# Performance work log

Measured on AMD Instinct MI355X. Metric: run time of the kernel, lower is better.

## Reference

```python
import jax, jax.numpy as jnp
import numpy as np
from jax import lax

B, C_IN, C_OUT, RES, K = 2, 16, 32, 64, 3


def setup_inputs() -> dict:
    key = jax.random.key(0)
    kx, km, kw = jax.random.split(key, 3)
    x = jax.random.normal(kx, (B, C_IN, RES, RES, RES), dtype=jnp.float32)
    # the rest are exactly zero -> drives the nonzero-voxel masking path
    keep = jax.random.bernoulli(km, 0.3, (B, 1, RES, RES, RES))
    x = x * keep.astype(jnp.float32)
    # weight matches nn.Parameter(torch.randn(1, out_ch, in_ch, k, k, k))
    weight = jax.random.normal(kw, (1, C_OUT, C_IN, K, K, K), dtype=jnp.float32)
    return {"x": x, "weight": weight}


def reference(x, weight):
    # SparseConv3d: output at voxel v (for each out channel) is
    #   sum_{i, dx, dy, dz} padded_x[i, v+offset] * W[o, i, offset+pad]
    # evaluated ONLY where x has any nonzero channel; zero elsewhere.
    # This is a 'same'-padded cross-correlation masked by voxel occupancy.
    w = weight[0]  # [O, I, k, k, k]
    out = lax.conv_general_dilated(
        x, w,
        window_strides=(1, 1, 1),
        padding="SAME",
        dimension_numbers=("NCDHW", "OIDHW", "NCDHW"),
    )  # [B, O, D, H, W]
    occ = jnp.any(x != 0, axis=1, keepdims=True)  # [B,1,D,H,W] nonzero-voxel mask
    return out * occ.astype(out.dtype)
```

## Files before the change

kernel.cpp:

```cpp
#include <hip/hip_runtime.h>

#define RES   64
#define RES2  4096
#define RES3  262144
#define CIN   16
#define COUT  32
#define NWH (27*CIN*COUT)

#define ROWB  1088
#define XT_BYTES (72*ROWB)
#define LDS_BYTES XT_BYTES

typedef _Float16 f16x8 __attribute__((ext_vector_type(8)));
typedef float   f32x16 __attribute__((ext_vector_type(16)));

static __device__ __forceinline__ unsigned int pack2(float v0, float v1) {
    _Float16 h0 = (_Float16)v0;
    _Float16 h1 = (_Float16)v1;
    unsigned short u0 = __builtin_bit_cast(unsigned short, h0);
    unsigned short u1 = __builtin_bit_cast(unsigned short, h1);
    return (unsigned int)u0 | ((unsigned int)u1 << 16);
}

__global__ __launch_bounds__(256) void wtrans_kernel(
    const float* __restrict__ w, _Float16* __restrict__ wtg) {
    int i = blockIdx.x * 256 + threadIdx.x;
    if (i >= NWH) return;
    int tap = i >> 9;
    int hi  = (i >> 8) & 1;
    int o   = (i >> 3) & 31;
    int c   = i & 7;
    wtg[i] = (_Float16)w[(o * CIN + hi * 8 + c) * 27 + tap];
}

__global__ __launch_bounds__(512, 4) void conv_kernel(
    const float* __restrict__ x, const char* __restrict__ wtgb,
    float* __restrict__ out) {

    extern __shared__ char smem[];
    char* xt = smem;

    int bid = blockIdx.x;
    int sb  = (bid & 7) * 64 + (bid >> 3);
    int b   = sb >> 8;
    int zt  = (sb >> 4) & 15;
    int yt  = sb & 15;
    int z0 = zt * 4, y0 = yt * 4;

    int tid  = threadIdx.x;
    int lane = tid & 63;
    int wv   = tid >> 6;
    int hi   = lane >> 5;
    int l31  = lane & 31;

    const float* xb = x + (size_t)b * CIN * RES3;
    const uint4 zz = make_uint4(0u, 0u, 0u, 0u);
    #pragma unroll
    for (int j = 0; j < 5; ++j) {
        int p = wv + j * 8;
        if (p >= 36) break;
        int iz = p / 6, iy = p - iz * 6;
        int gz = z0 + iz - 1, gy = y0 + iy - 1;
        char* d0 = xt + (p * 2) * ROWB;
        uint4 lo = zz, hh = zz;
        if (((unsigned)gz < 64u) && ((unsigned)gy < 64u)) {
            const float* sp = xb + gz * RES2 + gy * RES + lane;
            float v0  = sp[0];          float v1  = sp[RES3];
            float v2  = sp[2 * RES3];   float v3  = sp[3 * RES3];
            float v4  = sp[4 * RES3];   float v5  = sp[5 * RES3];
            float v6  = sp[6 * RES3];   float v7  = sp[7 * RES3];
            float v8  = sp[8 * RES3];   float v9  = sp[9 * RES3];
            float v10 = sp[10 * RES3];  float v11 = sp[11 * RES3];
            float v12 = sp[12 * RES3];  float v13 = sp[13 * RES3];
            float v14 = sp[14 * RES3];  float v15 = sp[15 * RES3];
            lo = make_uint4(pack2(v0, v1),  pack2(v2, v3),
                            pack2(v4, v5),  pack2(v6, v7));
            hh = make_uint4(pack2(v8, v9),  pack2(v10, v11),
                            pack2(v12, v13), pack2(v14, v15));
        }
        *(uint4*)(d0 + (lane + 1) * 16)        = lo;
        *(uint4*)(d0 + ROWB + (lane + 1) * 16) = hh;
        if (lane < 4) {
            int cz = (lane == 0) ? 0 : (64 + lane);
            *(uint4*)(d0 + cz * 16)        = zz;
            *(uint4*)(d0 + ROWB + cz * 16) = zz;
        }
    }
    __syncthreads();

    int oy  = wv & 3;
    int oz0 = (wv >> 2) * 2;

    const char* xbase = xt + hi * ROWB + l31 * 16;
    const char* wtab  = wtgb + hi * 512 + l31 * 16;

    f32x16 acc00 = {};
    f32x16 acc01 = {};
    f32x16 acc10 = {};
    f32x16 acc11 = {};

    #pragma unroll
    for (int g = 0; g < 3; ++g) {
        #pragma unroll
        for (int dyp = 0; dyp < 3; ++dyp) {
            const char* wp = wtab + (size_t)(g * 9 + dyp * 3) * 1024;
            f16x8 wf0 = *(const f16x8*)(wp);
            f16x8 wf1 = *(const f16x8*)(wp + 1024);
            f16x8 wf2 = *(const f16x8*)(wp + 2048);
            const char* xrow = xbase + (((oz0 + g) * 6 + (oy + dyp)) * 2) * ROWB;
            #pragma unroll
            for (int dxp = 0; dxp < 3; ++dxp) {
                f16x8 wf = (dxp == 0) ? wf0 : ((dxp == 1) ? wf1 : wf2);
                f16x8 bA0 = *(const f16x8*)(xrow + dxp * 16);
                f16x8 bA1 = *(const f16x8*)(xrow + 512 + dxp * 16);
                f16x8 bB0 = *(const f16x8*)(xrow + 12 * ROWB + dxp * 16);
                f16x8 bB1 = *(const f16x8*)(xrow + 12 * ROWB + 512 + dxp * 16);
                acc00 = __builtin_amdgcn_mfma_f32_32x32x16_f16(wf, bA0, acc00, 0, 0, 0);
                acc01 = __builtin_amdgcn_mfma_f32_32x32x16_f16(wf, bA1, acc01, 0, 0, 0);
                acc10 = __builtin_amdgcn_mfma_f32_32x32x16_f16(wf, bB0, acc10, 0, 0, 0);
                acc11 = __builtin_amdgcn_mfma_f32_32x32x16_f16(wf, bB1, acc11, 0, 0, 0);
            }
        }
    }

    unsigned occm[2][2];
    #pragma unroll
    for (int ozo = 0; ozo < 2; ++ozo) {
        int R = (((oz0 + ozo + 1) * 6) + (oy + 1)) * 2;
        #pragma unroll
        for (int xh = 0; xh < 2; ++xh) {
            const char* mp = xt + R * ROWB + (xh * 32 + l31 + 1) * 16;
            uint4 a = *(const uint4*)(mp);
            uint4 c = *(const uint4*)(mp + ROWB);
            occm[ozo][xh] = (a.x | a.y | a.z | a.w | c.x | c.y | c.z | c.w) & 0x7FFF7FFFu;
        }
    }
    bool oA0 = occm[0][0] != 0u, oA1 = occm[0][1] != 0u;
    bool oB0 = occm[1][0] != 0u, oB1 = occm[1][1] != 0u;

    size_t vaddrA = (size_t)(z0 + oz0) * RES2 + (y0 + oy) * RES + l31;
    size_t vaddrB = vaddrA + RES2;

    #pragma unroll
    for (int r = 0; r < 16; ++r) {
        int o = (r & 3) + 8 * (r >> 2) + 4 * hi;
        float* pl = out + ((size_t)(b * COUT + o) << 18);
        pl[vaddrA]      = oA0 ? acc00[r] : 0.0f;
        pl[vaddrA + 32] = oA1 ? acc01[r] : 0.0f;
        pl[vaddrB]      = oB0 ? acc10[r] : 0.0f;
        pl[vaddrB + 32] = oB1 ? acc11[r] : 0.0f;
    }
}

extern "C" void kernel_launch(void* const* d_in, const int* in_sizes, int n_in,
                              void* d_out, int out_size, void* d_ws, size_t ws_size,
                              hipStream_t stream) {
    const float* x = (const float*)d_in[0];
    const float* w = (const float*)d_in[1];
    float* out = (float*)d_out;

    _Float16* wtg = (_Float16*)d_ws;

    (void)hipFuncSetAttribute(reinterpret_cast<const void*>(conv_kernel),
                              hipFuncAttributeMaxDynamicSharedMemorySize, LDS_BYTES);

    wtrans_kernel<<<(NWH + 255) / 256, 256, 0, stream>>>(w, wtg);
    conv_kernel<<<512, 512, LDS_BYTES, stream>>>(x, (const char*)wtg, out);
}
```

Before: 101.9 us.

## Halve z-tile per block, preload all weights to registers, raise occupancy

Each block now covers 2 z-slices instead of 4, so the grid doubles to 1024 blocks and LDS per block shrinks to 48 rows. Each wave computes one output row with two accumulators instead of four. All 27 weight fragments are loaded into registers up front, and the MFMA loop runs at raised wave priority. Launch bounds go up to 6 blocks per CU to improve occupancy and latency hiding. The cost is more halo reloading, since each z-slice's input is staged by more blocks, and higher register pressure from the preloaded weights.

```diff
diff --git a/kernel.cpp b/kernel.cpp
--- a/kernel.cpp
+++ b/kernel.cpp
@@ -8,7 +8,7 @@
 #define NWH (27*CIN*COUT)
 
 #define ROWB  1088
-#define XT_BYTES (72*ROWB)
+#define XT_BYTES (48*ROWB)
 #define LDS_BYTES XT_BYTES
 
 typedef _Float16 f16x8 __attribute__((ext_vector_type(8)));
@@ -33,7 +33,7 @@
     wtg[i] = (_Float16)w[(o * CIN + hi * 8 + c) * 27 + tap];
 }
 
-__global__ __launch_bounds__(512, 4) void conv_kernel(
+__global__ __launch_bounds__(512, 6) void conv_kernel(
     const float* __restrict__ x, const char* __restrict__ wtgb,
     float* __restrict__ out) {
 
@@ -41,11 +41,11 @@
     char* xt = smem;
 
     int bid = blockIdx.x;
-    int sb  = (bid & 7) * 64 + (bid >> 3);
-    int b   = sb >> 8;
-    int zt  = (sb >> 4) & 15;
+    int sb  = (bid & 7) * 128 + (bid >> 3);
+    int b   = sb >> 9;
+    int zt  = (sb >> 4) & 31;
     int yt  = sb & 15;
-    int z0 = zt * 4, y0 = yt * 4;
+    int z0 = zt * 2, y0 = yt * 4;
 
     int tid  = threadIdx.x;
     int lane = tid & 63;
@@ -53,12 +53,16 @@
     int hi   = lane >> 5;
     int l31  = lane & 31;
 
+    const char* wtab = wtgb + hi * 512 + l31 * 16;
+    f16x8 wf[27];
+    #pragma unroll
+    for (int t = 0; t < 27; ++t) wf[t] = *(const f16x8*)(wtab + t * 1024);
+
     const float* xb = x + (size_t)b * CIN * RES3;
     const uint4 zz = make_uint4(0u, 0u, 0u, 0u);
     #pragma unroll
-    for (int j = 0; j < 5; ++j) {
-        int p = wv + j * 8;
-        if (p >= 36) break;
+    for (int j = 0; j < 3; ++j) {
+        int p = wv * 3 + j;
         int iz = p / 6, iy = p - iz * 6;
         int gz = z0 + iz - 1, gy = y0 + iy - 1;
         char* d0 = xt + (p * 2) * ROWB;
@@ -88,67 +92,55 @@
     }
     __syncthreads();
 
-    int oy  = wv & 3;
-    int oz0 = (wv >> 2) * 2;
+    int oy = wv & 3;
+    int oz = wv >> 2;
 
     const char* xbase = xt + hi * ROWB + l31 * 16;
-    const char* wtab  = wtgb + hi * 512 + l31 * 16;
 
-    f32x16 acc00 = {};
-    f32x16 acc01 = {};
-    f32x16 acc10 = {};
-    f32x16 acc11 = {};
+    f32x16 acc0 = {};
+    f32x16 acc1 = {};
 
+    __builtin_amdgcn_s_setprio(1);
     #pragma unroll
     for (int g = 0; g < 3; ++g) {
         #pragma unroll
         for (int dyp = 0; dyp < 3; ++dyp) {
-            const char* wp = wtab + (size_t)(g * 9 + dyp * 3) * 1024;
-            f16x8 wf0 = *(const f16x8*)(wp);
-            f16x8 wf1 = *(const f16x8*)(wp + 1024);
-            f16x8 wf2 = *(const f16x8*)(wp + 2048);
-            const char* xrow = xbase + (((oz0 + g) * 6 + (oy + dyp)) * 2) * ROWB;
+            const char* xrow = xbase + (((oz + g) * 6 + (oy + dyp)) * 2) * ROWB;
             #pragma unroll
             for (int dxp = 0; dxp < 3; ++dxp) {
-                f16x8 wf = (dxp == 0) ? wf0 : ((dxp == 1) ? wf1 : wf2);
-                f16x8 bA0 = *(const f16x8*)(xrow + dxp * 16);
-                f16x8 bA1 = *(const f16x8*)(xrow + 512 + dxp * 16);
-                f16x8 bB0 = *(const f16x8*)(xrow + 12 * ROWB + dxp * 16);
-                f16x8 bB1 = *(const f16x8*)(xrow + 12 * ROWB + 512 + dxp * 16);
-                acc00 = __builtin_amdgcn_mfma_f32_32x32x16_f16(wf, bA0, acc00, 0, 0, 0);
-                acc01 = __builtin_amdgcn_mfma_f32_32x32x16_f16(wf, bA1, acc01, 0, 0, 0);
-                acc10 = __builtin_amdgcn_mfma_f32_32x32x16_f16(wf, bB0, acc10, 0, 0, 0);
-                acc11 = __builtin_amdgcn_mfma_f32_32x32x16_f16(wf, bB1, acc11, 0, 0, 0);
+                f16x8 b0 = *(const f16x8*)(xrow + dxp * 16);
+                f16x8 b1 = *(const f16x8*)(xrow + 512 + dxp * 16);
+                acc0 = __builtin_amdgcn_mfma_f32_32x32x16_f16(
+                    wf[g * 9 + dyp * 3 + dxp], b0, acc0, 0, 0, 0);
+                acc1 = __builtin_amdgcn_mfma_f32_32x32x16_f16(
+                    wf[g * 9 + dyp * 3 + dxp], b1, acc1, 0, 0, 0);
             }
         }
     }
+    __builtin_amdgcn_s_setprio(0);
 
-    unsigned occm[2][2];
-    #pragma unroll
-    for (int ozo = 0; ozo < 2; ++ozo) {
-        int R = (((oz0 + ozo + 1) * 6) + (oy + 1)) * 2;
-        #pragma unroll
-        for (int xh = 0; xh < 2; ++xh) {
-            const char* mp = xt + R * ROWB + (xh * 32 + l31 + 1) * 16;
-            uint4 a = *(const uint4*)(mp);
-            uint4 c = *(const uint4*)(mp + ROWB);
-            occm[ozo][xh] = (a.x | a.y | a.z | a.w | c.x | c.y | c.z | c.w) & 0x7FFF7FFFu;
-        }
+    int R = ((oz + 1) * 6 + (oy + 1)) * 2;
+    unsigned m0, m1;
+    {
+        const char* mp = xt + R * ROWB + (l31 + 1) * 16;
+        uint4 a = *(const uint4*)(mp);
+        uint4 c = *(const uint4*)(mp + ROWB);
+        m0 = (a.x | a.y | a.z | a.w | c.x | c.y | c.z | c.w) & 0x7FFF7FFFu;
+        const char* mq = xt + R * ROWB + (32 + l31 + 1) * 16;
+        uint4 d = *(const uint4*)(mq);
+        uint4 e = *(const uint4*)(mq + ROWB);
+        m1 = (d.x | d.y | d.z | d.w | e.x | e.y | e.z | e.w) & 0x7FFF7FFFu;
     }
-    bool oA0 = occm[0][0] != 0u, oA1 = occm[0][1] != 0u;
-    bool oB0 = occm[1][0] != 0u, oB1 = occm[1][1] != 0u;
+    bool o0 = m0 != 0u, o1 = m1 != 0u;
 
-    size_t vaddrA = (size_t)(z0 + oz0) * RES2 + (y0 + oy) * RES + l31;
-    size_t vaddrB = vaddrA + RES2;
+    size_t vaddr = (size_t)(z0 + oz) * RES2 + (y0 + oy) * RES + l31;
 
     #pragma unroll
     for (int r = 0; r < 16; ++r) {
         int o = (r & 3) + 8 * (r >> 2) + 4 * hi;
         float* pl = out + ((size_t)(b * COUT + o) << 18);
-        pl[vaddrA]      = oA0 ? acc00[r] : 0.0f;
-        pl[vaddrA + 32] = oA1 ? acc01[r] : 0.0f;
-        pl[vaddrB]      = oB0 ? acc10[r] : 0.0f;
-        pl[vaddrB + 32] = oB1 ? acc11[r] : 0.0f;
+        pl[vaddr]      = o0 ? acc0[r] : 0.0f;
+        pl[vaddr + 32] = o1 ? acc1[r] : 0.0f;
     }
 }
 
@@ -165,5 +157,5 @@
                               hipFuncAttributeMaxDynamicSharedMemorySize, LDS_BYTES);
 
     wtrans_kernel<<<(NWH + 255) / 256, 256, 0, stream>>>(w, wtg);
-    conv_kernel<<<512, 512, LDS_BYTES, stream>>>(x, (const char*)wtg, out);
+    conv_kernel<<<1024, 512, LDS_BYTES, stream>>>(x, (const char*)wtg, out);
 }
```

After: 168.0 us. 1.65x slower.
